# Performance work log

Measured on AMD Instinct MI355X. Metric: run time of the kernel, lower is better.

The kernel has to match this reference:

```python
import jax, jax.numpy as jnp
import numpy as np

DIN, HID = 256, 512
SCALE = 1.0 / (64.0 * 6.0 ** 2)  # q / 2304, as in the torch code
NEG = 9e15


def setup_inputs() -> dict:
    key = jax.random.key(0)
    ks = jax.random.split(key, 8)
    B, N = 32, 1024
    x = jax.random.normal(ks[0], (B, N, DIN), dtype=jnp.float32)
    mask = jax.random.randint(ks[1], (B, N, N), 0, 2).astype(jnp.float32)
    lim = 1.0 / np.sqrt(DIN)
    Wv = jax.random.uniform(ks[2], (DIN, HID), minval=-lim, maxval=lim, dtype=jnp.float32)
    bv = jax.random.uniform(ks[3], (HID,), minval=-lim, maxval=lim, dtype=jnp.float32)
    Wk = jax.random.uniform(ks[4], (DIN, HID), minval=-lim, maxval=lim, dtype=jnp.float32)
    bk = jax.random.uniform(ks[5], (HID,), minval=-lim, maxval=lim, dtype=jnp.float32)
    Wq = jax.random.uniform(ks[6], (DIN, HID), minval=-lim, maxval=lim, dtype=jnp.float32)
    bq = jax.random.uniform(ks[7], (HID,), minval=-lim, maxval=lim, dtype=jnp.float32)
    return {"x": x, "mask": mask, "Wv": Wv, "bv": bv, "Wk": Wk, "bk": bk, "Wq": Wq, "bq": bq}


def reference(x, mask, Wv, bv, Wk, bk, Wq, bq):
    v = jax.nn.relu(x @ Wv + bv)                      # [B,N,H]
    q = jax.nn.relu(x @ Wq + bq)                      # [B,N,H]
    k = jax.nn.relu(x @ Wk + bk)                      # [B,N,H]
    scores = jnp.einsum('bnh,bmh->bnm', q * SCALE, k)  # [B,N,N]
    att = jax.nn.softmax(scores * mask - NEG * (1.0 - mask), axis=2)
    out = jax.nn.relu(jnp.einsum('bnm,bmh->bnh', att, v))
    return out
```

## Files before the change

### kernel.cpp

```cpp
#include <hip/hip_runtime.h>
#include <hip/hip_bf16.h>

#define DIN   256
#define HID   512
#define NBAT  32
#define NSEQ  1024
#define SCALEF (1.0f / 2304.0f)

typedef __attribute__((ext_vector_type(4))) float f32x4;
typedef __attribute__((ext_vector_type(8))) short bf16x8;
typedef unsigned short u16;

__device__ __forceinline__ u16 f2bf(float f) {
    union { float f; unsigned u; } v; v.f = f;
    unsigned r = v.u + 0x7fffu + ((v.u >> 16) & 1u);
    return (u16)(r >> 16);
}

__device__ __forceinline__ float bf2f(u16 b) {
    union { unsigned u; float f; } v; v.u = ((unsigned)b) << 16;
    return v.f;
}

__device__ __forceinline__ void g2lds16(const void* g, void* l) {
    __builtin_amdgcn_global_load_lds(
        (const __attribute__((address_space(1))) void*)g,
        (__attribute__((address_space(3))) void*)l,
        16, 0, 0);
}

__global__ __launch_bounds__(256) void prep_x(const float* __restrict__ x,
                                              u16* __restrict__ xb) {
    long i = (long)blockIdx.x * 256 + threadIdx.x;
    const long n4 = (long)NBAT * NSEQ * DIN / 4;
    if (i < n4) {
        float4 v = ((const float4*)x)[i];
        ushort4 o;
        o.x = f2bf(v.x); o.y = f2bf(v.y); o.z = f2bf(v.z); o.w = f2bf(v.w);
        ((ushort4*)xb)[i] = o;
    }
}

__global__ __launch_bounds__(256) void prep_w(
    const float* __restrict__ Wv, const float* __restrict__ bv,
    const float* __restrict__ Wk, const float* __restrict__ bk,
    const float* __restrict__ Wq, const float* __restrict__ bq,
    u16* __restrict__ Wtb, float* __restrict__ biascat) {
    int i = blockIdx.x * 256 + threadIdx.x;
    if (i < 1536 * 256) {
        int n = i >> 8, k = i & 255;
        const float* W = (n < 512) ? Wv : ((n < 1024) ? Wk : Wq);
        Wtb[i] = f2bf(W[k * 512 + (n & 511)]);
    }
    if (i < 1536) {
        biascat[i] = (i < 512) ? bv[i] : ((i < 1024) ? bk[i - 512] : bq[i - 1024]);
    }
}

__global__ __launch_bounds__(256) void gemm_qkv(
    const u16* __restrict__ A, const u16* __restrict__ Bt,
    u16* __restrict__ Cv, const float* __restrict__ bias) {
    __shared__ u16 lA[128 * 64];
    __shared__ u16 lB[128 * 64];
    const int t = threadIdx.x;
    const int lane = t & 63;
    const int w = t >> 6;
    const int bm = blockIdx.x * 128, bn = blockIdx.y * 128;

    const int srow = t >> 3;
    const int csrc = ((t & 7) ^ (srow & 7)) * 8;
    const u16* gA0 = A + (long)(bm + srow) * 256 + csrc;
    const u16* gB0 = Bt + (long)(bn + srow) * 256 + csrc;

    const int wr = (w >> 1) * 64, wc = (w & 1) * 64;
    const int frow = lane & 15;
    const int kq = lane >> 4;

    f32x4 acc[4][4] = {};

    for (int k0 = 0; k0 < 256; k0 += 64) {
        __syncthreads();
#pragma unroll
        for (int p = 0; p < 4; ++p) {
            g2lds16(gA0 + (long)p * 32 * 256 + k0, &lA[p * 2048 + t * 8]);
            g2lds16(gB0 + (long)p * 32 * 256 + k0, &lB[p * 2048 + t * 8]);
        }
        __syncthreads();
#pragma unroll
        for (int kk = 0; kk < 2; ++kk) {
            const int sc = ((kk * 4 + kq) ^ (frow & 7)) * 8;
            bf16x8 af[4], bfr[4];
#pragma unroll
            for (int i = 0; i < 4; ++i)
                af[i] = *(const bf16x8*)&lA[(wr + i * 16 + frow) * 64 + sc];
#pragma unroll
            for (int j = 0; j < 4; ++j)
                bfr[j] = *(const bf16x8*)&lB[(wc + j * 16 + frow) * 64 + sc];
#pragma unroll
            for (int i = 0; i < 4; ++i)
#pragma unroll
                for (int j = 0; j < 4; ++j)
                    acc[i][j] = __builtin_amdgcn_mfma_f32_16x16x32_bf16(
                        af[i], bfr[j], acc[i][j], 0, 0, 0);
        }
    }

    const int crow0 = bm + wr + (lane >> 4) * 4;
    const int ccol0 = bn + wc + (lane & 15);
#pragma unroll
    for (int i = 0; i < 4; ++i)
#pragma unroll
        for (int j = 0; j < 4; ++j) {
            int col = ccol0 + j * 16;
#pragma unroll
            for (int r = 0; r < 4; ++r) {
                int row = crow0 + i * 16 + r;
                float v = acc[i][j][r] + bias[col];
                v = v > 0.0f ? v : 0.0f;
                if (col >= 1024) v *= SCALEF;
                Cv[(long)row * 1536 + col] = f2bf(v);
            }
        }
}

__global__ __launch_bounds__(256) void transpose_v(const u16* __restrict__ qkv,
                                                   u16* __restrict__ vt) {
    __shared__ u16 tile[64][72];
    const int t = threadIdx.x;
    const int b = blockIdx.z;
    const int n0 = blockIdx.x * 64, h0 = blockIdx.y * 64;
    const u16* src = qkv + (long)(b * NSEQ + n0) * 1536 + h0;
#pragma unroll
    for (int it = 0; it < 2; ++it) {
        int n = (t >> 3) + it * 32;
        int hc = (t & 7) * 8;
        *(bf16x8*)&tile[n][hc] = *(const bf16x8*)&src[(long)n * 1536 + hc];
    }
    __syncthreads();
    u16* dst = vt + ((long)b * HID + h0) * NSEQ + n0;
#pragma unroll
    for (int it = 0; it < 2; ++it) {
        int h = (t >> 3) + it * 32;
        int nc = (t & 7) * 8;
        bf16x8 v;
#pragma unroll
        for (int j = 0; j < 8; ++j) v[j] = (short)tile[nc + j][h];
        *(bf16x8*)&dst[(long)h * NSEQ + nc] = v;
    }
}

__global__ __launch_bounds__(256, 2) void fused_attn(
    const u16* __restrict__ qkv, const u16* __restrict__ vt,
    const float* __restrict__ mask, float* __restrict__ out) {
    __shared__ u16 lQ[64 * 64];
    __shared__ u16 lK[128 * 64];
    __shared__ u16 lP[64 * 136];
    __shared__ u16 lV[512 * 32];
    __shared__ float lred[4][64];

    const int t = threadIdx.x;
    const int lane = t & 63;
    const int w = t >> 6;

    const int f = (int)blockIdx.x;
    const int j = f >> 3;
    const int b = (f & 7) + 8 * (j >> 4);
    const int qt = j & 15;
    const int n0 = qt * 64;

    const u16* qb = qkv + (long)b * NSEQ * 1536 + 1024;
    const u16* kb = qkv + (long)b * NSEQ * 1536 + 512;
    const u16* vb = vt + (long)b * HID * NSEQ;
    const float* mb = mask + (long)b * NSEQ * NSEQ;

    const int frow = lane & 15;
    const int kq = lane >> 4;

    const int srow = t >> 3;
    const int csrc = ((t & 7) ^ (srow & 7)) * 8;
    const int vrow = t >> 2;
    const int vchunk = t & 3;

    f32x4 o_acc[4][8] = {};
    float lsum[16] = {};

    for (int kvt = 0; kvt < 8; ++kvt) {
        const int kv0 = kvt * 128;
        f32x4 s_acc[4][2] = {};

        for (int d0 = 0; d0 < 512; d0 += 64) {
            __syncthreads();
#pragma unroll
            for (int p = 0; p < 2; ++p)
                g2lds16(qb + (long)(n0 + p * 32 + srow) * 1536 + d0 + csrc,
                        &lQ[p * 2048 + t * 8]);
#pragma unroll
            for (int p = 0; p < 4; ++p)
                g2lds16(kb + (long)(kv0 + p * 32 + srow) * 1536 + d0 + csrc,
                        &lK[p * 2048 + t * 8]);
            __syncthreads();
#pragma unroll
            for (int kk = 0; kk < 2; ++kk) {
                const int sc = ((kk * 4 + kq) ^ (frow & 7)) * 8;
                bf16x8 af[4], bf[2];
#pragma unroll
                for (int i = 0; i < 4; ++i)
                    af[i] = *(const bf16x8*)&lQ[(i * 16 + frow) * 64 + sc];
#pragma unroll
                for (int jq = 0; jq < 2; ++jq)
                    bf[jq] = *(const bf16x8*)&lK[(w * 32 + jq * 16 + frow) * 64 + sc];
#pragma unroll
                for (int i = 0; i < 4; ++i)
#pragma unroll
                    for (int jq = 0; jq < 2; ++jq)
                        s_acc[i][jq] = __builtin_amdgcn_mfma_f32_16x16x32_bf16(
                            af[i], bf[jq], s_acc[i][jq], 0, 0, 0);
            }
        }

        __syncthreads();
#pragma unroll
        for (int i = 0; i < 4; ++i)
#pragma unroll
            for (int jq = 0; jq < 2; ++jq) {
                const int col = w * 32 + jq * 16 + frow;
#pragma unroll
                for (int r = 0; r < 4; ++r) {
                    const int row = i * 16 + (lane >> 4) * 4 + r;
                    float mv = mb[(long)(n0 + row) * NSEQ + kv0 + col];
                    float p = mv * __expf(s_acc[i][jq][r]);
                    u16 pb = f2bf(p);
                    lP[row * 136 + col] = pb;
                    lsum[i * 4 + r] += bf2f(pb);
                }
            }

        for (int ks = 0; ks < 4; ++ks) {
            __syncthreads();
#pragma unroll
            for (int p = 0; p < 8; ++p) {
                const int vr = p * 64 + vrow;
                const int vc = (vchunk ^ (vr & 3)) * 8;
                g2lds16(vb + (long)vr * NSEQ + kv0 + ks * 32 + vc,
                        &lV[p * 2048 + t * 8]);
            }
            __syncthreads();
            bf16x8 ap[4];
#pragma unroll
            for (int i = 0; i < 4; ++i)
                ap[i] = *(const bf16x8*)&lP[(i * 16 + frow) * 136 + ks * 32 + kq * 8];
#pragma unroll
            for (int jo = 0; jo < 8; ++jo) {
                const int h = w * 128 + jo * 16 + frow;
                bf16x8 bv8 = *(const bf16x8*)&lV[h * 32 + ((kq ^ (h & 3)) * 8)];
#pragma unroll
                for (int i = 0; i < 4; ++i)
                    o_acc[i][jo] = __builtin_amdgcn_mfma_f32_16x16x32_bf16(
                        ap[i], bv8, o_acc[i][jo], 0, 0, 0);
            }
        }
    }

#pragma unroll
    for (int s = 0; s < 16; ++s) {
        lsum[s] += __shfl_xor(lsum[s], 1);
        lsum[s] += __shfl_xor(lsum[s], 2);
        lsum[s] += __shfl_xor(lsum[s], 4);
        lsum[s] += __shfl_xor(lsum[s], 8);
    }
    if ((lane & 15) == 0) {
#pragma unroll
        for (int i = 0; i < 4; ++i)
#pragma unroll
            for (int r = 0; r < 4; ++r)
                lred[w][i * 16 + (lane >> 4) * 4 + r] = lsum[i * 4 + r];
    }
    __syncthreads();
    float linv[16];
#pragma unroll
    for (int i = 0; i < 4; ++i)
#pragma unroll
        for (int r = 0; r < 4; ++r) {
            const int row = i * 16 + (lane >> 4) * 4 + r;
            linv[i * 4 + r] = 1.0f /
                (lred[0][row] + lred[1][row] + lred[2][row] + lred[3][row]);
        }
#pragma unroll
    for (int i = 0; i < 4; ++i)
#pragma unroll
        for (int jo = 0; jo < 8; ++jo) {
            const int col = w * 128 + jo * 16 + frow;
#pragma unroll
            for (int r = 0; r < 4; ++r) {
                const int row = n0 + i * 16 + (lane >> 4) * 4 + r;
                float v = o_acc[i][jo][r] * linv[i * 4 + r];
                out[((long)b * NSEQ + row) * HID + col] = v > 0.0f ? v : 0.0f;
            }
        }
}

extern "C" void kernel_launch(void* const* d_in, const int* in_sizes, int n_in,
                              void* d_out, int out_size, void* d_ws, size_t ws_size,
                              hipStream_t stream) {
    const float* x    = (const float*)d_in[0];
    const float* mask = (const float*)d_in[1];
    const float* Wv   = (const float*)d_in[2];
    const float* bv   = (const float*)d_in[3];
    const float* Wk   = (const float*)d_in[4];
    const float* bk   = (const float*)d_in[5];
    const float* Wq   = (const float*)d_in[6];
    const float* bq   = (const float*)d_in[7];
    float* out = (float*)d_out;

    char* ws = (char*)d_ws;
    u16*   xb      = (u16*)ws;   ws += (long)NBAT * NSEQ * DIN * 2;
    u16*   Wtb     = (u16*)ws;   ws += (long)1536 * 256 * 2;
    float* biascat = (float*)ws; ws += 1536 * 4;
    u16*   qkv     = (u16*)ws;   ws += (long)NBAT * NSEQ * 1536 * 2;
    u16*   vt      = (u16*)ws;   ws += (long)NBAT * HID * NSEQ * 2;

    prep_x<<<8192, 256, 0, stream>>>(x, xb);
    prep_w<<<1536, 256, 0, stream>>>(Wv, bv, Wk, bk, Wq, bq, Wtb, biascat);

    gemm_qkv<<<dim3(256, 12), 256, 0, stream>>>(xb, Wtb, qkv, biascat);

    transpose_v<<<dim3(16, 8, NBAT), 256, 0, stream>>>(qkv, vt);

    fused_attn<<<NBAT * 16, 256, 0, stream>>>(qkv, vt, mask, out);
}
```

Measured before the change: 441.6 us.

## Double-buffer Q/K LDS staging and read V fragments directly from global

Q and K tiles now go through two LDS buffers, and the next tile's load is issued before computing on the current one. This hides global-to-LDS latency and removes one barrier per depth step. The V tile no longer goes through LDS: each wave reads its bf16x8 B-fragments straight from the transposed V in global memory, which removes eight LDS staging loads and two barriers per sub-step. The cost is uncoalesced or repeated global reads for V, which now depend on L2/L1 hits, and lower LDS use that may change occupancy.

```diff
diff --git a/kernel.cpp b/kernel.cpp
--- a/kernel.cpp
+++ b/kernel.cpp
@@ -152,10 +152,9 @@
 __global__ __launch_bounds__(256, 2) void fused_attn(
     const u16* __restrict__ qkv, const u16* __restrict__ vt,
     const float* __restrict__ mask, float* __restrict__ out) {
-    __shared__ u16 lQ[64 * 64];
-    __shared__ u16 lK[128 * 64];
+    __shared__ u16 lQ[2][64 * 64];
+    __shared__ u16 lK[2][128 * 64];
     __shared__ u16 lP[64 * 136];
-    __shared__ u16 lV[512 * 32];
     __shared__ float lred[4][64];
 
     const int t = threadIdx.x;
@@ -165,8 +164,7 @@
     const int f = (int)blockIdx.x;
     const int j = f >> 3;
     const int b = (f & 7) + 8 * (j >> 4);
-    const int qt = j & 15;
-    const int n0 = qt * 64;
+    const int n0 = (j & 15) * 64;
 
     const u16* qb = qkv + (long)b * NSEQ * 1536 + 1024;
     const u16* kb = qkv + (long)b * NSEQ * 1536 + 512;
@@ -178,47 +176,56 @@
 
     const int srow = t >> 3;
     const int csrc = ((t & 7) ^ (srow & 7)) * 8;
-    const int vrow = t >> 2;
-    const int vchunk = t & 3;
 
     f32x4 o_acc[4][8] = {};
     float lsum[16] = {};
+
+    auto stageQK = [&](int kvt, int d0, int bufi) {
+#pragma unroll
+        for (int p = 0; p < 2; ++p)
+            g2lds16(qb + (long)(n0 + p * 32 + srow) * 1536 + d0 + csrc,
+                    &lQ[bufi][p * 2048 + t * 8]);
+#pragma unroll
+        for (int p = 0; p < 4; ++p)
+            g2lds16(kb + (long)(kvt * 128 + p * 32 + srow) * 1536 + d0 + csrc,
+                    &lK[bufi][p * 2048 + t * 8]);
+    };
+
+    stageQK(0, 0, 0);
+    __syncthreads();
+    int cur = 0;
 
     for (int kvt = 0; kvt < 8; ++kvt) {
         const int kv0 = kvt * 128;
         f32x4 s_acc[4][2] = {};
 
-        for (int d0 = 0; d0 < 512; d0 += 64) {
-            __syncthreads();
-#pragma unroll
-            for (int p = 0; p < 2; ++p)
-                g2lds16(qb + (long)(n0 + p * 32 + srow) * 1536 + d0 + csrc,
-                        &lQ[p * 2048 + t * 8]);
-#pragma unroll
-            for (int p = 0; p < 4; ++p)
-                g2lds16(kb + (long)(kv0 + p * 32 + srow) * 1536 + d0 + csrc,
-                        &lK[p * 2048 + t * 8]);
-            __syncthreads();
+        for (int ds = 0; ds < 8; ++ds) {
+            if (!(kvt == 7 && ds == 7)) {
+                const int nk = (ds < 7) ? kvt : kvt + 1;
+                const int nd = (ds < 7) ? (ds + 1) * 64 : 0;
+                stageQK(nk, nd, cur ^ 1);
+            }
 #pragma unroll
             for (int kk = 0; kk < 2; ++kk) {
                 const int sc = ((kk * 4 + kq) ^ (frow & 7)) * 8;
-                bf16x8 af[4], bf[2];
+                bf16x8 af[4], bfk[2];
 #pragma unroll
                 for (int i = 0; i < 4; ++i)
-                    af[i] = *(const bf16x8*)&lQ[(i * 16 + frow) * 64 + sc];
+                    af[i] = *(const bf16x8*)&lQ[cur][(i * 16 + frow) * 64 + sc];
 #pragma unroll
                 for (int jq = 0; jq < 2; ++jq)
-                    bf[jq] = *(const bf16x8*)&lK[(w * 32 + jq * 16 + frow) * 64 + sc];
+                    bfk[jq] = *(const bf16x8*)&lK[cur][(w * 32 + jq * 16 + frow) * 64 + sc];
 #pragma unroll
                 for (int i = 0; i < 4; ++i)
 #pragma unroll
                     for (int jq = 0; jq < 2; ++jq)
                         s_acc[i][jq] = __builtin_amdgcn_mfma_f32_16x16x32_bf16(
-                            af[i], bf[jq], s_acc[i][jq], 0, 0, 0);
-            }
-        }
-
-        __syncthreads();
+                            af[i], bfk[jq], s_acc[i][jq], 0, 0, 0);
+            }
+            __syncthreads();
+            cur ^= 1;
+        }
+
 #pragma unroll
         for (int i = 0; i < 4; ++i)
 #pragma unroll
@@ -234,17 +241,10 @@
                     lsum[i * 4 + r] += bf2f(pb);
                 }
             }
-
+        __syncthreads();
+
+#pragma unroll
         for (int ks = 0; ks < 4; ++ks) {
-            __syncthreads();
-#pragma unroll
-            for (int p = 0; p < 8; ++p) {
-                const int vr = p * 64 + vrow;
-                const int vc = (vchunk ^ (vr & 3)) * 8;
-                g2lds16(vb + (long)vr * NSEQ + kv0 + ks * 32 + vc,
-                        &lV[p * 2048 + t * 8]);
-            }
-            __syncthreads();
             bf16x8 ap[4];
 #pragma unroll
             for (int i = 0; i < 4; ++i)
@@ -252,13 +252,14 @@
 #pragma unroll
             for (int jo = 0; jo < 8; ++jo) {
                 const int h = w * 128 + jo * 16 + frow;
-                bf16x8 bv8 = *(const bf16x8*)&lV[h * 32 + ((kq ^ (h & 3)) * 8)];
+                bf16x8 bv8 = *(const bf16x8*)&vb[(long)h * NSEQ + kv0 + ks * 32 + kq * 8];
 #pragma unroll
                 for (int i = 0; i < 4; ++i)
                     o_acc[i][jo] = __builtin_amdgcn_mfma_f32_16x16x32_bf16(
                         ap[i], bv8, o_acc[i][jo], 0, 0, 0);
             }
         }
+        __syncthreads();
     }
 
 #pragma unroll
```

After: 590.7 us. +33.8%, slower.
